# Kernel optimization log

Measured on AMD Instinct MI355X. Metric: run time of the kernel, lower is better.

## Reference

```python
import jax, jax.numpy as jnp
import numpy as np

TOP_K = 2  # num_experts_per_tok


def setup_inputs() -> dict:
    key = jax.random.key(0)
    ks = jax.random.split(key, 5)
    B, S, D, M, E = 4, 2048, 2048, 2048, 8
    x = jax.random.normal(ks[0], (B, S, D), dtype=jnp.float32)
    gate_kernel = jax.random.normal(ks[1], (D, E), dtype=jnp.float32) / np.sqrt(D)
    wi_0 = jax.random.normal(ks[2], (E, D, M), dtype=jnp.float32) / np.sqrt(D)
    wi_1 = jax.random.normal(ks[3], (E, D, M), dtype=jnp.float32) / np.sqrt(D)
    wo = jax.random.normal(ks[4], (E, M, D), dtype=jnp.float32) / np.sqrt(M)
    return {"x": x, "gate_kernel": gate_kernel, "wi_0": wi_0, "wi_1": wi_1, "wo": wo}


def reference(x, gate_kernel, wi_0, wi_1, wo):
    E = gate_kernel.shape[-1]
    # Gate logits: (B, S, E)
    gate_logits = jnp.einsum("bsd,de->bse", x, gate_kernel)
    # Top-k routing, then softmax over the selected experts' logits
    top_k_weights, top_k_indices = jax.lax.top_k(gate_logits, TOP_K)
    top_k_weights = jax.nn.softmax(top_k_weights.astype(jnp.float32), axis=-1).astype(x.dtype)
    # Dense combine weights per expert: (B, S, E)
    combine_w = jnp.sum(
        jax.nn.one_hot(top_k_indices, E, dtype=x.dtype) * top_k_weights[..., None], axis=-2
    )
    # Grouped GEMM (dense-masked form, as in MaxText dense_matmul path)
    h0 = jnp.einsum("bsd,edm->bsem", x, wi_0)  # (B, S, E, M)
    h1 = jnp.einsum("bsd,edm->bsem", x, wi_1)
    h = jax.nn.silu(h0) * h1 * combine_w[..., None]
    out = jnp.einsum("bsem,emd->bsd", h, wo)  # (B, S, D)
    return out
```

## Files before the change

kernel.cpp:

```cpp
#include <hip/hip_runtime.h>
#include <hip/hip_bf16.h>
#include <stdint.h>

#define TT   8192
#define DD   2048
#define MM   2048
#define NE   8

typedef float f32x4 __attribute__((ext_vector_type(4)));
typedef short s16x8 __attribute__((ext_vector_type(8)));
typedef unsigned int u32;

static __device__ __forceinline__ short f2bf(float f) {
  __hip_bfloat16 h = __float2bfloat16(f);
  short s;
  __builtin_memcpy(&s, &h, 2);
  return s;
}

static __device__ __forceinline__ void gload_lds16(const short* g, short* lds) {
  __builtin_amdgcn_global_load_lds(
      (const __attribute__((address_space(1))) u32*)g,
      (__attribute__((address_space(3))) u32*)lds, 16, 0, 0);
}

__global__ __launch_bounds__(256) void cvt_kernel(const float* __restrict__ in,
                                                  short* __restrict__ out, size_t n) {
  size_t idx = ((size_t)blockIdx.x * 256 + threadIdx.x) * 8;
  size_t stride = (size_t)gridDim.x * 256 * 8;
  for (size_t i = idx; i < n; i += stride) {
    f32x4 a = *(const f32x4*)(in + i);
    f32x4 b = *(const f32x4*)(in + i + 4);
    s16x8 v;
    v[0]=f2bf(a[0]); v[1]=f2bf(a[1]); v[2]=f2bf(a[2]); v[3]=f2bf(a[3]);
    v[4]=f2bf(b[0]); v[5]=f2bf(b[1]); v[6]=f2bf(b[2]); v[7]=f2bf(b[3]);
    *(s16x8*)(out + i) = v;
  }
}

__global__ __launch_bounds__(256) void tcvt_kernel(
    const float* __restrict__ w0, const float* __restrict__ w1, const float* __restrict__ w2,
    short* __restrict__ o0, short* __restrict__ o1, short* __restrict__ o2) {
  __shared__ short tile[64][65];
  const int bz = blockIdx.z;
  const float* in; short* out;
  if (bz < 8)       { in = w0; out = o0; }
  else if (bz < 16) { in = w1; out = o1; }
  else              { in = w2; out = o2; }
  const int ex = bz & 7;
  const float* src = in + (size_t)ex * DD * MM;
  short* dst = out + (size_t)ex * DD * MM;
  const int r0 = blockIdx.y * 64;
  const int c0 = blockIdx.x * 64;
  const int t = threadIdx.x;
  const int rr = t >> 4, cc = (t & 15) * 4;
  #pragma unroll
  for (int i = 0; i < 4; i++) {
    int row = rr + i * 16;
    f32x4 v = *(const f32x4*)(src + (size_t)(r0 + row) * MM + c0 + cc);
    tile[cc + 0][row] = f2bf(v[0]);
    tile[cc + 1][row] = f2bf(v[1]);
    tile[cc + 2][row] = f2bf(v[2]);
    tile[cc + 3][row] = f2bf(v[3]);
  }
  __syncthreads();
  const int orow = t >> 2, c8 = (t & 3) * 16;
  s16x8 v0, v1;
  #pragma unroll
  for (int i = 0; i < 8; i++) { v0[i] = tile[orow][c8 + i]; v1[i] = tile[orow][c8 + 8 + i]; }
  short* dp = dst + (size_t)(c0 + orow) * DD + r0 + c8;
  *(s16x8*)(dp) = v0;
  *(s16x8*)(dp + 8) = v1;
}

__global__ __launch_bounds__(256) void gate_kernel(const float* __restrict__ x,
    const float* __restrict__ gk, int* __restrict__ counts,
    int* __restrict__ tkidx, float* __restrict__ tkw) {
  int t = blockIdx.x;
  const float* xr = x + (size_t)t * DD;
  float acc[NE];
  #pragma unroll
  for (int e = 0; e < NE; e++) acc[e] = 0.f;
  for (int d = threadIdx.x; d < DD; d += 256) {
    float xv = xr[d];
    const float* g = gk + (size_t)d * NE;
    #pragma unroll
    for (int e = 0; e < NE; e++) acc[e] += xv * g[e];
  }
  #pragma unroll
  for (int e = 0; e < NE; e++) {
    #pragma unroll
    for (int off = 32; off >= 1; off >>= 1)
      acc[e] += __shfl_xor(acc[e], off, 64);
  }
  __shared__ float red[4][NE];
  int wid = threadIdx.x >> 6;
  int lane = threadIdx.x & 63;
  if (lane == 0) {
    #pragma unroll
    for (int e = 0; e < NE; e++) red[wid][e] = acc[e];
  }
  __syncthreads();
  if (threadIdx.x == 0) {
    float l[NE];
    #pragma unroll
    for (int e = 0; e < NE; e++) l[e] = red[0][e] + red[1][e] + red[2][e] + red[3][e];
    int i1 = 0; float v1 = l[0];
    #pragma unroll
    for (int e = 1; e < NE; e++) if (l[e] > v1) { v1 = l[e]; i1 = e; }
    int i2 = -1; float v2 = -1e30f;
    #pragma unroll
    for (int e = 0; e < NE; e++) if (e != i1 && l[e] > v2) { v2 = l[e]; i2 = e; }
    float p = __expf(v2 - v1);
    float inv = 1.f / (1.f + p);
    tkidx[t*2]   = i1; tkidx[t*2+1] = i2;
    tkw[t*2]     = inv; tkw[t*2+1]  = p * inv;
    atomicAdd(&counts[i1], 1);
    atomicAdd(&counts[i2], 1);
  }
}

__global__ __launch_bounds__(256) void scatter_kernel(const int* __restrict__ counts,
    int* __restrict__ offsets, const int* __restrict__ tkidx,
    const float* __restrict__ tkw, int* __restrict__ ltok, float* __restrict__ lwt,
    int* __restrict__ slots) {
  __shared__ int soff[NE];
  __shared__ int scur[NE];
  if (threadIdx.x == 0) {
    int s = 0;
    for (int e = 0; e < NE; e++) { offsets[e] = s; soff[e] = s; s += counts[e]; scur[e] = 0; }
    offsets[NE] = s;
  }
  __syncthreads();
  for (int i = threadIdx.x; i < TT * 2; i += 256) {
    int e = tkidx[i];
    int pos = atomicAdd(&scur[e], 1);
    int dst = soff[e] + pos;
    ltok[dst] = i >> 1;
    lwt[dst]  = tkw[i];
    slots[i]  = dst;
  }
}

__global__ __launch_bounds__(256) void combine_kernel(const float* __restrict__ comb,
    const int* __restrict__ slots, float* __restrict__ out) {
  const int t = blockIdx.x;
  const int s0 = slots[2 * t], s1 = slots[2 * t + 1];
  const f32x4* p0 = (const f32x4*)(comb + (size_t)s0 * DD);
  const f32x4* p1 = (const f32x4*)(comb + (size_t)s1 * DD);
  f32x4* po = (f32x4*)(out + (size_t)t * DD);
  #pragma unroll
  for (int i = 0; i < 2; i++) {
    int idx = threadIdx.x + i * 256;
    po[idx] = p0[idx] + p1[idx];
  }
}

__device__ __forceinline__ void find_seg(const int* __restrict__ offsets, int tile, int bm,
                                         int& e, int& row0, int& rows, int& seg) {
  e = -1; row0 = 0; rows = 0; seg = 0;
  int accT = 0, prev = offsets[0];
  #pragma unroll
  for (int i = 0; i < NE; i++) {
    int nxt = offsets[i+1];
    int cnt = nxt - prev;
    int nt = (cnt + bm - 1) / bm;
    if (e < 0 && tile < accT + nt) { e = i; row0 = (tile - accT) * bm; rows = cnt; seg = prev; }
    accT += nt; prev = nxt;
  }
}

__device__ __forceinline__ void xcd_map(int& tile, int& nyi) {
  const int nx = gridDim.x;
  const int nwg = nx * gridDim.y;
  const int bid = blockIdx.y * nx + blockIdx.x;
  const int cpx = nwg >> 3;
  const int s = (bid & 7) * cpx + (bid >> 3);
  tile = s % nx;
  nyi  = s / nx;
}

#define MAXT_F 136

__global__ __launch_bounds__(256, 2) void gemm1_fast(
    const short* __restrict__ xbf,
    const short* __restrict__ w0t, const short* __restrict__ w1t,
    const int* __restrict__ offsets,
    const int* __restrict__ ltok, const float* __restrict__ lwt,
    short* __restrict__ hbuf) {
  __shared__ short As[128 * 64];
  __shared__ short B0s[128 * 64];
  __shared__ short B1s[128 * 64];
  __shared__ float w_s[128];

  int tile, nyi;
  xcd_map(tile, nyi);
  const int n0 = nyi * 128;
  int e, row0, rows, seg;
  find_seg(offsets, tile, 128, e, row0, rows, seg);
  if (e < 0) return;

  const int tid = threadIdx.x;
  const int lane = tid & 63, wid = tid >> 6;
  if (tid < 128) {
    int gr = row0 + tid;
    w_s[tid] = (gr < rows) ? lwt[seg + gr] : 0.f;
  }

  const int swz = ((lane & 7) ^ (lane >> 3)) * 8;
  const short* abase[4];
  const short* b0base[4];
  const short* b1base[4];
  #pragma unroll
  for (int c = 0; c < 4; c++) {
    int chunk = wid * 4 + c;
    int r = chunk * 8 + (lane >> 3);
    int gr = row0 + r; if (gr >= rows) gr = rows - 1;
    int tok = ltok[seg + gr];
    abase[c]  = xbf + (size_t)tok * DD + swz;
    int n = n0 + r;
    b0base[c] = w0t + ((size_t)e * MM + n) * DD + swz;
    b1base[c] = w1t + ((size_t)e * MM + n) * DD + swz;
  }

  const int wr = wid >> 1, wc = wid & 1;
  const int lr = lane & 15;
  const int kq = (lane >> 4) * 8;

  f32x4 acc0[4][4], acc1[4][4];
  #pragma unroll
  for (int i = 0; i < 4; i++)
    #pragma unroll
    for (int j = 0; j < 4; j++) { acc0[i][j] = 0.f; acc1[i][j] = 0.f; }

  for (int k0 = 0; k0 < DD; k0 += 64) {
    #pragma unroll
    for (int c = 0; c < 4; c++) {
      int chunk = wid * 4 + c;
      gload_lds16(abase[c]  + k0, As  + chunk * 512);
      gload_lds16(b0base[c] + k0, B0s + chunk * 512);
      gload_lds16(b1base[c] + k0, B1s + chunk * 512);
    }
    __syncthreads();

    #pragma unroll
    for (int ks = 0; ks < 2; ks++) {
      s16x8 a[4], b0[4], b1[4];
      #pragma unroll
      for (int mi = 0; mi < 4; mi++) {
        int row = wr * 64 + mi * 16 + lr;
        int koff = (ks * 32 + kq) ^ ((row & 7) * 8);
        a[mi] = *(const s16x8*)&As[row * 64 + koff];
      }
      #pragma unroll
      for (int ni = 0; ni < 4; ni++) {
        int row = wc * 64 + ni * 16 + lr;
        int koff = (ks * 32 + kq) ^ ((row & 7) * 8);
        b0[ni] = *(const s16x8*)&B0s[row * 64 + koff];
        b1[ni] = *(const s16x8*)&B1s[row * 64 + koff];
      }
      #pragma unroll
      for (int mi = 0; mi < 4; mi++)
        #pragma unroll
        for (int ni = 0; ni < 4; ni++) {
          acc0[mi][ni] = __builtin_amdgcn_mfma_f32_16x16x32_bf16(a[mi], b0[ni], acc0[mi][ni], 0, 0, 0);
          acc1[mi][ni] = __builtin_amdgcn_mfma_f32_16x16x32_bf16(a[mi], b1[ni], acc1[mi][ni], 0, 0, 0);
        }
    }
    __syncthreads();
  }

  const int lq = lane >> 4;
  #pragma unroll
  for (int mi = 0; mi < 4; mi++) {
    #pragma unroll
    for (int jj = 0; jj < 4; jj++) {
      int r = wr * 64 + mi * 16 + lq * 4 + jj;
      int gr = row0 + r;
      if (gr < rows) {
        float wgt = w_s[r];
        size_t hrow = (size_t)(seg + gr) * MM + n0;
        #pragma unroll
        for (int ni = 0; ni < 4; ni++) {
          int c = wc * 64 + ni * 16 + lr;
          float g = acc0[mi][ni][jj];
          float u = acc1[mi][ni][jj];
          float act = g / (1.f + __expf(-g));
          hbuf[hrow + c] = f2bf(act * u * wgt);
        }
      }
    }
  }
}

__global__ __launch_bounds__(256, 2) void gemm2_fast(
    const short* __restrict__ hbuf,
    const short* __restrict__ wot,
    const int* __restrict__ offsets,
    float* __restrict__ comb) {
  __shared__ short As[128 * 64];
  __shared__ short Bs[128 * 64];

  int tile, nyi;
  xcd_map(tile, nyi);
  const int n0 = nyi * 128;
  int e, row0, rows, seg;
  find_seg(offsets, tile, 128, e, row0, rows, seg);
  if (e < 0) return;

  const int tid = threadIdx.x;
  const int lane = tid & 63, wid = tid >> 6;

  const int swz = ((lane & 7) ^ (lane >> 3)) * 8;
  const short* abase[4];
  const short* bbase[4];
  #pragma unroll
  for (int c = 0; c < 4; c++) {
    int chunk = wid * 4 + c;
    int r = chunk * 8 + (lane >> 3);
    int gr = row0 + r; if (gr >= rows) gr = rows - 1;
    abase[c] = hbuf + (size_t)(seg + gr) * MM + swz;
    int n = n0 + r;
    bbase[c] = wot + ((size_t)e * DD + n) * MM + swz;
  }

  const int wr = wid >> 1, wc = wid & 1;
  const int lr = lane & 15;
  const int kq = (lane >> 4) * 8;

  f32x4 acc[4][4];
  #pragma unroll
  for (int i = 0; i < 4; i++)
    #pragma unroll
    for (int j = 0; j < 4; j++) acc[i][j] = 0.f;

  for (int k0 = 0; k0 < MM; k0 += 64) {
    #pragma unroll
    for (int c = 0; c < 4; c++) {
      int chunk = wid * 4 + c;
      gload_lds16(abase[c] + k0, As + chunk * 512);
      gload_lds16(bbase[c] + k0, Bs + chunk * 512);
    }
    __syncthreads();

    #pragma unroll
    for (int ks = 0; ks < 2; ks++) {
      s16x8 a[4], b[4];
      #pragma unroll
      for (int mi = 0; mi < 4; mi++) {
        int row = wr * 64 + mi * 16 + lr;
        int koff = (ks * 32 + kq) ^ ((row & 7) * 8);
        a[mi] = *(const s16x8*)&As[row * 64 + koff];
      }
      #pragma unroll
      for (int ni = 0; ni < 4; ni++) {
        int row = wc * 64 + ni * 16 + lr;
        int koff = (ks * 32 + kq) ^ ((row & 7) * 8);
        b[ni] = *(const s16x8*)&Bs[row * 64 + koff];
      }
      #pragma unroll
      for (int mi = 0; mi < 4; mi++)
        #pragma unroll
        for (int ni = 0; ni < 4; ni++)
          acc[mi][ni] = __builtin_amdgcn_mfma_f32_16x16x32_bf16(a[mi], b[ni], acc[mi][ni], 0, 0, 0);
    }
    __syncthreads();
  }

  const int lq = lane >> 4;
  #pragma unroll
  for (int mi = 0; mi < 4; mi++) {
    #pragma unroll
    for (int jj = 0; jj < 4; jj++) {
      int r = wr * 64 + mi * 16 + lq * 4 + jj;
      int gr = row0 + r;
      if (gr < rows) {
        size_t orow = (size_t)(seg + gr) * DD + n0;
        #pragma unroll
        for (int ni = 0; ni < 4; ni++) {
          int c = wc * 64 + ni * 16 + lr;
          comb[orow + c] = acc[mi][ni][jj];
        }
      }
    }
  }
}

extern "C" void kernel_launch(void* const* d_in, const int* in_sizes, int n_in,
                              void* d_out, int out_size, void* d_ws, size_t ws_size,
                              hipStream_t stream) {
  const float* x   = (const float*)d_in[0];
  const float* gk  = (const float*)d_in[1];
  const float* wi0 = (const float*)d_in[2];
  const float* wi1 = (const float*)d_in[3];
  const float* wo  = (const float*)d_in[4];
  float* out = (float*)d_out;

  char* w = (char*)d_ws;
  int*   counts  = (int*)(w);
  int*   offsets = (int*)(w + 256);
  int*   tkidx   = (int*)(w + 1024);
  float* tkw     = (float*)(w + 1024 + 65536);
  int*   ltok    = (int*)(w + 1024 + 2*65536);
  float* lwt     = (float*)(w + 1024 + 3*65536);
  int*   slots   = (int*)(w + 1024 + 4*65536);
  short* xbf  = (short*)(w + 524288);
  short* hbuf = xbf + (size_t)TT * DD;
  short* w0t  = hbuf + (size_t)2 * TT * MM;
  short* w1t  = w0t + (size_t)NE * DD * MM;
  short* wot  = w1t + (size_t)NE * DD * MM;
  float* comb = (float*)w0t;

  hipMemsetAsync(counts, 0, 64, stream);

  cvt_kernel<<<1024, 256, 0, stream>>>(x, xbf, (size_t)TT * DD);
  gate_kernel<<<TT, 256, 0, stream>>>(x, gk, counts, tkidx, tkw);
  scatter_kernel<<<1, 256, 0, stream>>>(counts, offsets, tkidx, tkw, ltok, lwt, slots);
  tcvt_kernel<<<dim3(MM/64, DD/64, 24), 256, 0, stream>>>(wi0, wi1, wo, w0t, w1t, wot);

  gemm1_fast<<<dim3(MAXT_F, MM/128), 256, 0, stream>>>(xbf, w0t, w1t, offsets, ltok, lwt, hbuf);
  gemm2_fast<<<dim3(MAXT_F, DD/128), 256, 0, stream>>>(hbuf, wot, offsets, comb);
  combine_kernel<<<TT, 256, 0, stream>>>(comb, slots, out);
}
```

Before: 911.1 us.

## Fuse x bf16 conversion into gate kernel and widen gemm2 N tile

Removes the separate x-to-bf16 conversion kernel by having the gate kernel convert and write each token row while it already holds x in registers, saving one full read of x and a launch. The down-projection GEMM now computes a 128x256 output tile per block using two B tiles, so each A tile loaded from hbuf is reused twice, halving A traffic and the grid size. This doubles accumulator registers and LDS use, which may lower occupancy under the launch_bounds(256,2) hint, and the grid y dimension must still match xcd_map's assumptions.

```diff
diff --git a/kernel.cpp b/kernel.cpp
--- a/kernel.cpp
+++ b/kernel.cpp
@@ -22,20 +22,6 @@
   __builtin_amdgcn_global_load_lds(
       (const __attribute__((address_space(1))) u32*)g,
       (__attribute__((address_space(3))) u32*)lds, 16, 0, 0);
-}
-
-__global__ __launch_bounds__(256) void cvt_kernel(const float* __restrict__ in,
-                                                  short* __restrict__ out, size_t n) {
-  size_t idx = ((size_t)blockIdx.x * 256 + threadIdx.x) * 8;
-  size_t stride = (size_t)gridDim.x * 256 * 8;
-  for (size_t i = idx; i < n; i += stride) {
-    f32x4 a = *(const f32x4*)(in + i);
-    f32x4 b = *(const f32x4*)(in + i + 4);
-    s16x8 v;
-    v[0]=f2bf(a[0]); v[1]=f2bf(a[1]); v[2]=f2bf(a[2]); v[3]=f2bf(a[3]);
-    v[4]=f2bf(b[0]); v[5]=f2bf(b[1]); v[6]=f2bf(b[2]); v[7]=f2bf(b[3]);
-    *(s16x8*)(out + i) = v;
-  }
 }
 
 __global__ __launch_bounds__(256) void tcvt_kernel(
@@ -75,15 +61,24 @@
 
 __global__ __launch_bounds__(256) void gate_kernel(const float* __restrict__ x,
     const float* __restrict__ gk, int* __restrict__ counts,
-    int* __restrict__ tkidx, float* __restrict__ tkw) {
+    int* __restrict__ tkidx, float* __restrict__ tkw, short* __restrict__ xbf) {
   int t = blockIdx.x;
   const float* xr = x + (size_t)t * DD;
+  const int d0 = threadIdx.x * 8;
+  f32x4 a = *(const f32x4*)(xr + d0);
+  f32x4 b = *(const f32x4*)(xr + d0 + 4);
+  s16x8 v;
+  v[0]=f2bf(a[0]); v[1]=f2bf(a[1]); v[2]=f2bf(a[2]); v[3]=f2bf(a[3]);
+  v[4]=f2bf(b[0]); v[5]=f2bf(b[1]); v[6]=f2bf(b[2]); v[7]=f2bf(b[3]);
+  *(s16x8*)(xbf + (size_t)t * DD + d0) = v;
+
   float acc[NE];
   #pragma unroll
   for (int e = 0; e < NE; e++) acc[e] = 0.f;
-  for (int d = threadIdx.x; d < DD; d += 256) {
-    float xv = xr[d];
-    const float* g = gk + (size_t)d * NE;
+  #pragma unroll
+  for (int j = 0; j < 8; j++) {
+    float xv = (j < 4) ? a[j] : b[j - 4];
+    const float* g = gk + (size_t)(d0 + j) * NE;
     #pragma unroll
     for (int e = 0; e < NE; e++) acc[e] += xv * g[e];
   }
@@ -299,11 +294,12 @@
     const int* __restrict__ offsets,
     float* __restrict__ comb) {
   __shared__ short As[128 * 64];
-  __shared__ short Bs[128 * 64];
+  __shared__ short B0s[128 * 64];
+  __shared__ short B1s[128 * 64];
 
   int tile, nyi;
   xcd_map(tile, nyi);
-  const int n0 = nyi * 128;
+  const int n0 = nyi * 256;
   int e, row0, rows, seg;
   find_seg(offsets, tile, 128, e, row0, rows, seg);
   if (e < 0) return;
@@ -313,39 +309,41 @@
 
   const int swz = ((lane & 7) ^ (lane >> 3)) * 8;
   const short* abase[4];
-  const short* bbase[4];
+  const short* b0base[4];
+  const short* b1base[4];
   #pragma unroll
   for (int c = 0; c < 4; c++) {
     int chunk = wid * 4 + c;
     int r = chunk * 8 + (lane >> 3);
     int gr = row0 + r; if (gr >= rows) gr = rows - 1;
     abase[c] = hbuf + (size_t)(seg + gr) * MM + swz;
-    int n = n0 + r;
-    bbase[c] = wot + ((size_t)e * DD + n) * MM + swz;
+    b0base[c] = wot + ((size_t)e * DD + n0 + r) * MM + swz;
+    b1base[c] = wot + ((size_t)e * DD + n0 + 128 + r) * MM + swz;
   }
 
   const int wr = wid >> 1, wc = wid & 1;
   const int lr = lane & 15;
   const int kq = (lane >> 4) * 8;
 
-  f32x4 acc[4][4];
+  f32x4 acc0[4][4], acc1[4][4];
   #pragma unroll
   for (int i = 0; i < 4; i++)
     #pragma unroll
-    for (int j = 0; j < 4; j++) acc[i][j] = 0.f;
+    for (int j = 0; j < 4; j++) { acc0[i][j] = 0.f; acc1[i][j] = 0.f; }
 
   for (int k0 = 0; k0 < MM; k0 += 64) {
     #pragma unroll
     for (int c = 0; c < 4; c++) {
       int chunk = wid * 4 + c;
-      gload_lds16(abase[c] + k0, As + chunk * 512);
-      gload_lds16(bbase[c] + k0, Bs + chunk * 512);
+      gload_lds16(abase[c]  + k0, As  + chunk * 512);
+      gload_lds16(b0base[c] + k0, B0s + chunk * 512);
+      gload_lds16(b1base[c] + k0, B1s + chunk * 512);
     }
     __syncthreads();
 
     #pragma unroll
     for (int ks = 0; ks < 2; ks++) {
-      s16x8 a[4], b[4];
+      s16x8 a[4], b0[4], b1[4];
       #pragma unroll
       for (int mi = 0; mi < 4; mi++) {
         int row = wr * 64 + mi * 16 + lr;
@@ -356,13 +354,16 @@
       for (int ni = 0; ni < 4; ni++) {
         int row = wc * 64 + ni * 16 + lr;
         int koff = (ks * 32 + kq) ^ ((row & 7) * 8);
-        b[ni] = *(const s16x8*)&Bs[row * 64 + koff];
+        b0[ni] = *(const s16x8*)&B0s[row * 64 + koff];
+        b1[ni] = *(const s16x8*)&B1s[row * 64 + koff];
       }
       #pragma unroll
       for (int mi = 0; mi < 4; mi++)
         #pragma unroll
-        for (int ni = 0; ni < 4; ni++)
-          acc[mi][ni] = __builtin_amdgcn_mfma_f32_16x16x32_bf16(a[mi], b[ni], acc[mi][ni], 0, 0, 0);
+        for (int ni = 0; ni < 4; ni++) {
+          acc0[mi][ni] = __builtin_amdgcn_mfma_f32_16x16x32_bf16(a[mi], b0[ni], acc0[mi][ni], 0, 0, 0);
+          acc1[mi][ni] = __builtin_amdgcn_mfma_f32_16x16x32_bf16(a[mi], b1[ni], acc1[mi][ni], 0, 0, 0);
+        }
     }
     __syncthreads();
   }
@@ -379,7 +380,8 @@
         #pragma unroll
         for (int ni = 0; ni < 4; ni++) {
           int c = wc * 64 + ni * 16 + lr;
-          comb[orow + c] = acc[mi][ni][jj];
+          comb[orow + c] = acc0[mi][ni][jj];
+          comb[orow + 128 + c] = acc1[mi][ni][jj];
         }
       }
     }
@@ -413,12 +415,11 @@
 
   hipMemsetAsync(counts, 0, 64, stream);
 
-  cvt_kernel<<<1024, 256, 0, stream>>>(x, xbf, (size_t)TT * DD);
-  gate_kernel<<<TT, 256, 0, stream>>>(x, gk, counts, tkidx, tkw);
+  gate_kernel<<<TT, 256, 0, stream>>>(x, gk, counts, tkidx, tkw, xbf);
   scatter_kernel<<<1, 256, 0, stream>>>(counts, offsets, tkidx, tkw, ltok, lwt, slots);
   tcvt_kernel<<<dim3(MM/64, DD/64, 24), 256, 0, stream>>>(wi0, wi1, wo, w0t, w1t, wot);
 
   gemm1_fast<<<dim3(MAXT_F, MM/128), 256, 0, stream>>>(xbf, w0t, w1t, offsets, ltok, lwt, hbuf);
-  gemm2_fast<<<dim3(MAXT_F, DD/128), 256, 0, stream>>>(hbuf, wot, offsets, comb);
+  gemm2_fast<<<dim3(MAXT_F, DD/256), 256, 0, stream>>>(hbuf, wot, offsets, comb);
   combine_kernel<<<TT, 256, 0, stream>>>(comb, slots, out);
 }
```

Result: no change. 904.0 us (-0.8%).
